# Optimization experiments

Measured on AMD Instinct MI355X. Metric: run time of the kernel, lower is better.

The kernel has to match this reference:

```python
import jax, jax.numpy as jnp
import numpy as np

B, T, D, E, H = 4, 2048, 1024, 4, 8
EPS = 1e-5


def _uniform(k, shape, bound):
    return jax.random.uniform(k, shape, jnp.float32, -bound, bound)


def setup_inputs() -> dict:
    key = jax.random.key(0)
    ks = jax.random.split(key, 12)
    wb = np.sqrt(6.0 / D) / np.sqrt(6.0)  # kaiming_uniform(a=sqrt5) bound ~ 1/sqrt(D)... keep simple
    wb = 1.0 / np.sqrt(D)
    return {
        "x": jax.random.normal(ks[0], (B, T, D), jnp.float32),
        "router_prob": jax.random.uniform(ks[1], (B, T, E), jnp.float32),
        "norm_w": jnp.ones((D,), jnp.float32),
        "norm_b": jnp.zeros((D,), jnp.float32),
        "q_w": _uniform(ks[2], (D, D), wb),
        "q_b": _uniform(ks[3], (D,), wb),
        "k_w": _uniform(ks[4], (D, D), wb),
        "k_b": _uniform(ks[5], (D,), wb),
        "v_w": _uniform(ks[6], (D, D), wb),
        "v_b": _uniform(ks[7], (D,), wb),
        "o_w": _uniform(ks[8], (D, D), wb),
        "o_b": _uniform(ks[9], (D,), wb),
    }


def _layernorm(x, w, b):
    mu = jnp.mean(x, axis=-1, keepdims=True)
    var = jnp.mean(jnp.square(x - mu), axis=-1, keepdims=True)
    return (x - mu) * jax.lax.rsqrt(var + EPS) * w + b


def reference(x, router_prob, norm_w, norm_b, q_w, q_b, k_w, k_b, v_w, v_b, o_w, o_b):
    e_cnt = router_prob.shape[2]
    b, t, d = x.shape
    n = t // e_cnt
    h = H
    scale = d ** (-0.5)  # note: original uses model_dim**-0.5, not head_dim

    qs, ks_, vs = [], [], []
    for e in range(e_cnt):
        xe = x[:, e * n:(e + 1) * n, :]
        xn = _layernorm(xe, norm_w, norm_b)
        m = d // (2 ** e)
        xm = xn[..., :m]  # [b, n, m] matryoshka slice
        # F.linear(xm, W[:, :m], bias): out = xm @ W[:, :m]^T + b -> [b, n, d]
        qs.append(jnp.einsum('bnm,dm->bnd', xm, q_w[:, :m]) + q_b)
        ks_.append(jnp.einsum('bnm,dm->bnd', xm, k_w[:, :m]) + k_b)
        vs.append(jnp.einsum('bnm,dm->bnd', xm, v_w[:, :m]) + v_b)
    q = jnp.concatenate(qs, axis=1)
    k = jnp.concatenate(ks_, axis=1)
    v = jnp.concatenate(vs, axis=1)

    dh = d // h
    q = q.reshape(b, t, h, dh).transpose(0, 2, 1, 3)  # b h t dh
    k = k.reshape(b, t, h, dh).transpose(0, 2, 1, 3)
    v = v.reshape(b, t, h, dh).transpose(0, 2, 1, 3)

    attn = jnp.einsum('bhqd,bhkd->bhqk', q, k) * scale
    attn = jax.nn.softmax(attn, axis=-1)  # dropout = identity in eval
    attn_out = jnp.einsum('bhqk,bhkd->bhqd', attn, v)
    attn_out = attn_out.transpose(0, 2, 1, 3).reshape(b, t, d)

    outs = []
    for e in range(e_cnt):
        sl = slice(e * n, (e + 1) * n)
        m = d // (2 ** e)
        xm = attn_out[:, sl, :m]
        out = jnp.einsum('bnm,om->bno', xm, o_w[:m, :m]) + o_b[:m]  # [b, n, m]
        pad = d - m
        if pad:
            out = jnp.pad(out, ((0, 0), (0, 0), (0, pad)))
        outs.append(out + x[:, sl, :])
    return jnp.concatenate(outs, axis=1)
```

## Files before the change

### kernel.cpp

```cpp
#include <hip/hip_runtime.h>
#include <hip/hip_bf16.h>

#define DEV static __device__ __forceinline__

typedef __attribute__((ext_vector_type(4))) float f32x4;
typedef __attribute__((ext_vector_type(8))) short s16x8;
typedef __attribute__((ext_vector_type(4))) unsigned int u32x4;

constexpr int Bn = 4, Tn = 2048, Dn = 1024, Hn = 8, DH = 128;
constexpr float EPSF = 1e-5f;
constexpr float QSCALE = 0.0450842200277801f;

DEV unsigned short f2bf(float f) {
    unsigned int u = __float_as_uint(f);
    u += 0x7FFF + ((u >> 16) & 1);
    return (unsigned short)(u >> 16);
}

DEV f32x4 mfma16(s16x8 a, s16x8 b, f32x4 c) {
    return __builtin_amdgcn_mfma_f32_16x16x32_bf16(a, b, c, 0, 0, 0);
}

DEV float ex2(float x) {
    float r;
    asm("v_exp_f32 %0, %1" : "=v"(r) : "v"(x));
    return r;
}

DEV unsigned int cvtpk(float lo, float hi) {
    unsigned int r;
    asm("v_cvt_pk_bf16_f32 %0, %1, %2" : "=v"(r) : "v"(lo), "v"(hi));
    return r;
}

typedef __attribute__((address_space(1))) const unsigned int GU32;
typedef __attribute__((address_space(3))) unsigned int LU32;
DEV void gload16(const void* g, void* l) {
    __builtin_amdgcn_global_load_lds((GU32*)g, (LU32*)l, 16, 0, 0);
}

__global__ void cvt_w_kernel(const float* __restrict__ qw, const float* __restrict__ kw,
                             const float* __restrict__ vw, const float* __restrict__ ow,
                             unsigned short* __restrict__ dst) {
    int idx = blockIdx.x * blockDim.x + threadIdx.x;
    const int total = 4 * Dn * Dn;
    for (; idx < total; idx += gridDim.x * blockDim.x) {
        int sel = idx >> 20;
        int off = idx & (Dn * Dn - 1);
        const float* src = sel == 0 ? qw : sel == 1 ? kw : sel == 2 ? vw : ow;
        dst[idx] = f2bf(src[off]);
    }
}

__global__ __launch_bounds__(256) void ln_kernel(const float* __restrict__ x,
                                                 const float* __restrict__ w,
                                                 const float* __restrict__ b,
                                                 unsigned short* __restrict__ xn) {
    int tok = blockIdx.x;
    int tid = threadIdx.x;
    const float* xp = x + (size_t)tok * Dn;
    float4 v = ((const float4*)xp)[tid];
    float s = v.x + v.y + v.z + v.w;
    float q = v.x * v.x + v.y * v.y + v.z * v.z + v.w * v.w;
    for (int off = 32; off; off >>= 1) {
        s += __shfl_xor(s, off);
        q += __shfl_xor(q, off);
    }
    __shared__ float red[8];
    __shared__ float stats[2];
    int wid = tid >> 6, lane = tid & 63;
    if (lane == 0) { red[wid] = s; red[4 + wid] = q; }
    __syncthreads();
    if (tid == 0) {
        float ts = red[0] + red[1] + red[2] + red[3];
        float tq = red[4] + red[5] + red[6] + red[7];
        float mu = ts / Dn;
        float var = tq / Dn - mu * mu;
        stats[0] = mu;
        stats[1] = rsqrtf(var + EPSF);
    }
    __syncthreads();
    float mu = stats[0], rs = stats[1];
    int c = tid * 4;
    ushort4 o;
    o.x = f2bf((v.x - mu) * rs * w[c + 0] + b[c + 0]);
    o.y = f2bf((v.y - mu) * rs * w[c + 1] + b[c + 1]);
    o.z = f2bf((v.z - mu) * rs * w[c + 2] + b[c + 2]);
    o.w = f2bf((v.w - mu) * rs * w[c + 3] + b[c + 3]);
    ((ushort4*)(xn + (size_t)tok * Dn))[tid] = o;
}

__global__ __launch_bounds__(256) void qkv_gemm(const unsigned short* __restrict__ xn,
                                                const unsigned short* __restrict__ wmat,
                                                const float* __restrict__ qb_,
                                                const float* __restrict__ kb_,
                                                const float* __restrict__ vb_,
                                                unsigned short* __restrict__ outq,
                                                unsigned short* __restrict__ outk,
                                                unsigned short* __restrict__ vt) {
    int rowbase = blockIdx.x * 128;
    int colbase = blockIdx.y * 128;
    int matid = blockIdx.z;
    const unsigned short* W = wmat + (size_t)matid * Dn * Dn;
    const float* bias = matid == 0 ? qb_ : matid == 1 ? kb_ : vb_;
    float oscale = matid == 0 ? QSCALE : 1.0f;
    int e = (rowbase & (Tn - 1)) >> 9;
    int m = Dn >> e;
    int nt = m >> 5;

    __shared__ alignas(16) unsigned short At[4][128 * 32];
    __shared__ alignas(16) unsigned short Bt[4][128 * 32];

    int tid = threadIdx.x;
    int lane = tid & 63, wv = tid >> 6;
    int wr = (wv >> 1) * 64, wc = (wv & 1) * 64;
    int fr = lane & 15, fg = lane >> 4;
    int srow = tid >> 2, scol = (tid & 3) * 8;
    const unsigned short* ga0 = xn + (size_t)(rowbase + srow) * Dn + scol;
    const unsigned short* ga1 = xn + (size_t)(rowbase + 64 + srow) * Dn + scol;
    const unsigned short* gb0 = W + (size_t)(colbase + srow) * Dn + scol;
    const unsigned short* gb1 = W + (size_t)(colbase + 64 + srow) * Dn + scol;

    f32x4 acc[4][4] = {};

    auto STAGE = [&](int tt) {
        int buf = tt & 3, kk = tt * 32;
        gload16(ga0 + kk, &At[buf][tid * 8]);
        gload16(ga1 + kk, &At[buf][2048 + tid * 8]);
        gload16(gb0 + kk, &Bt[buf][tid * 8]);
        gload16(gb1 + kk, &Bt[buf][2048 + tid * 8]);
    };

    STAGE(0);
    if (nt > 1) STAGE(1);

    for (int t = 0; t < nt; t++) {
        if (t + 1 < nt) { asm volatile("s_waitcnt vmcnt(4)" ::: "memory"); }
        else            { asm volatile("s_waitcnt vmcnt(0)" ::: "memory"); }
        __builtin_amdgcn_s_barrier();
        if (t + 2 < nt) STAGE(t + 2);
        int cur = t & 3;
        s16x8 a[4], b[4];
        #pragma unroll
        for (int i = 0; i < 4; i++) a[i] = *(const s16x8*)&At[cur][(wr + i * 16 + fr) * 32 + fg * 8];
        #pragma unroll
        for (int j = 0; j < 4; j++) b[j] = *(const s16x8*)&Bt[cur][(wc + j * 16 + fr) * 32 + fg * 8];
        #pragma unroll
        for (int i = 0; i < 4; i++)
            #pragma unroll
            for (int j = 0; j < 4; j++) acc[i][j] = mfma16(a[i], b[j], acc[i][j]);
    }

    if (matid == 2) {
        #pragma unroll
        for (int i = 0; i < 4; i++)
            #pragma unroll
            for (int j = 0; j < 4; j++) {
                int col = colbase + wc + j * 16 + fr;
                float bv = bias[col];
                int row0 = rowbase + wr + i * 16 + fg * 4;
                int bb = row0 >> 11, tl = row0 & (Tn - 1);
                int w32 = tl & 31;
                int tlp = (tl & ~31) | (((w32 >> 2) & 3) * 8 + ((w32 >> 4) & 1) * 4);
                size_t base = (((size_t)bb * Hn + (col >> 7)) * DH + (col & (DH - 1))) * Tn + tlp;
                ushort4 o;
                o.x = f2bf(acc[i][j][0] + bv);
                o.y = f2bf(acc[i][j][1] + bv);
                o.z = f2bf(acc[i][j][2] + bv);
                o.w = f2bf(acc[i][j][3] + bv);
                *(ushort4*)&vt[base] = o;
            }
    } else {
        unsigned short* out = matid == 0 ? outq : outk;
        #pragma unroll
        for (int i = 0; i < 4; i++)
            #pragma unroll
            for (int j = 0; j < 4; j++) {
                int col = colbase + wc + j * 16 + fr;
                float bv = bias[col];
                #pragma unroll
                for (int r = 0; r < 4; r++) {
                    int row = rowbase + wr + i * 16 + fg * 4 + r;
                    out[(size_t)row * Dn + col] = f2bf((acc[i][j][r] + bv) * oscale);
                }
            }
    }
}

__global__ __launch_bounds__(256, 2) void attn_kernel(const unsigned short* __restrict__ Q,
                                                      const unsigned short* __restrict__ K,
                                                      const unsigned short* __restrict__ VT,
                                                      unsigned short* __restrict__ AO) {
    int f = blockIdx.x;
    int qi = f >> 5;
    int bh = f & 31;
    int b = bh >> 3, h = bh & 7;
    int qbase = qi * 128;
    int tid = threadIdx.x;
    int wv = tid >> 6, lane = tid & 63;
    int fr = lane & 15, fg = lane >> 4;

    __shared__ alignas(16) unsigned short Kt[2][64 * 128];
    __shared__ alignas(16) unsigned short Vt[2][128 * 64];

    s16x8 bq[2][4];
    #pragma unroll
    for (int hh = 0; hh < 2; hh++) {
        const size_t qr = ((size_t)b * Tn + qbase + wv * 32 + hh * 16 + fr) * Dn + h * DH;
        #pragma unroll
        for (int c = 0; c < 4; c++) bq[hh][c] = *(const s16x8*)&Q[qr + c * 32 + fg * 8];
    }

    const s16x8 ones = {(short)0x3F80, (short)0x3F80, (short)0x3F80, (short)0x3F80,
                        (short)0x3F80, (short)0x3F80, (short)0x3F80, (short)0x3F80};

    f32x4 acc[2][9] = {};
    float m_run[2] = {-1e30f, -1e30f};

    const unsigned short* Kbase = K + (size_t)b * Tn * Dn + h * DH;
    const unsigned short* Vbase = VT + ((size_t)b * Hn + h) * DH * Tn;

    int k_row_lo = tid >> 4, k_chk = tid & 15;
    int v_row_lo = tid >> 3, v_chk = tid & 7;

    auto STAGE = [&](int t, int buf) {
        int kb = t * 64;
        #pragma unroll
        for (int p = 0; p < 4; p++) {
            int row = p * 16 + k_row_lo;
            int chunk = k_chk ^ (row & 7);
            gload16(Kbase + (size_t)(kb + row) * Dn + chunk * 8,
                    &Kt[buf][p * 2048 + tid * 8]);
        }
        #pragma unroll
        for (int p = 0; p < 4; p++) {
            int row = p * 32 + v_row_lo;
            int chunk = v_chk ^ (row & 7);
            gload16(Vbase + (size_t)row * Tn + kb + chunk * 8,
                    &Vt[buf][p * 2048 + tid * 8]);
        }
    };

    STAGE(0, 0);
    __syncthreads();

    for (int t = 0; t < Tn / 64; t++) {
        int cur = t & 1;
        if (t < Tn / 64 - 1) STAGE(t + 1, cur ^ 1);

        const unsigned short* KtC = &Kt[cur][0];
        const unsigned short* VtC = &Vt[cur][0];

        f32x4 s[2][4] = {};
        __builtin_amdgcn_s_setprio(1);
        #pragma unroll
        for (int c = 0; c < 4; c++) {
            #pragma unroll
            for (int kt = 0; kt < 4; kt++) {
                s16x8 ak = *(const s16x8*)&KtC[(kt * 16 + fr) * 128 +
                                               (((c * 4 + fg) ^ (fr & 7)) * 8)];
                s[0][kt] = mfma16(ak, bq[0][c], s[0][kt]);
                s[1][kt] = mfma16(ak, bq[1][c], s[1][kt]);
            }
        }
        __builtin_amdgcn_s_setprio(0);

        float mx[2];
        #pragma unroll
        for (int hh = 0; hh < 2; hh++) {
            float v = s[hh][0][0];
            #pragma unroll
            for (int kt = 0; kt < 4; kt++)
                #pragma unroll
                for (int r = 0; r < 4; r++) v = fmaxf(v, s[hh][kt][r]);
            v = fmaxf(v, __shfl_xor(v, 16));
            v = fmaxf(v, __shfl_xor(v, 32));
            mx[hh] = v;
        }

        if (!__all(mx[0] - m_run[0] <= 8.0f && mx[1] - m_run[1] <= 8.0f)) {
            #pragma unroll
            for (int hh = 0; hh < 2; hh++) {
                float mnew = fmaxf(m_run[hh], mx[hh]);
                float fsc = ex2(m_run[hh] - mnew);
                float fw[4];
                #pragma unroll
                for (int r = 0; r < 4; r++) fw[r] = __shfl(fsc, fg * 4 + r);
                #pragma unroll
                for (int n = 0; n < 9; n++)
                    #pragma unroll
                    for (int r = 0; r < 4; r++) acc[hh][n][r] *= fw[r];
                m_run[hh] = mnew;
            }
        }

        s16x8 pa[2][2];
        #pragma unroll
        for (int hh = 0; hh < 2; hh++) {
            float p[16];
            #pragma unroll
            for (int kt = 0; kt < 4; kt++)
                #pragma unroll
                for (int r = 0; r < 4; r++) p[kt * 4 + r] = ex2(s[hh][kt][r] - m_run[hh]);
            #pragma unroll
            for (int ks = 0; ks < 2; ks++) {
                u32x4 pw;
                pw.x = cvtpk(p[ks * 8 + 0], p[ks * 8 + 1]);
                pw.y = cvtpk(p[ks * 8 + 2], p[ks * 8 + 3]);
                pw.z = cvtpk(p[ks * 8 + 4], p[ks * 8 + 5]);
                pw.w = cvtpk(p[ks * 8 + 6], p[ks * 8 + 7]);
                pa[hh][ks] = __builtin_bit_cast(s16x8, pw);
            }
        }

        __builtin_amdgcn_s_setprio(1);
        #pragma unroll
        for (int ks = 0; ks < 2; ks++) {
            #pragma unroll
            for (int n = 0; n < 8; n++) {
                int row = n * 16 + fr;
                s16x8 bv = *(const s16x8*)&VtC[row * 64 +
                                               (((ks * 4 + fg) ^ (fr & 7)) * 8)];
                acc[0][n] = mfma16(pa[0][ks], bv, acc[0][n]);
                acc[1][n] = mfma16(pa[1][ks], bv, acc[1][n]);
            }
            acc[0][8] = mfma16(pa[0][ks], ones, acc[0][8]);
            acc[1][8] = mfma16(pa[1][ks], ones, acc[1][8]);
        }
        __builtin_amdgcn_s_setprio(0);
        __syncthreads();
    }

    #pragma unroll
    for (int hh = 0; hh < 2; hh++) {
        float rl[4];
        #pragma unroll
        for (int r = 0; r < 4; r++) rl[r] = 1.0f / acc[hh][8][r];
        size_t orow0 = ((size_t)b * Tn + qbase + wv * 32 + hh * 16) * Dn + h * DH;
        for (int n = 0; n < 8; n++)
            for (int r = 0; r < 4; r++) {
                float v = acc[hh][n][r] * rl[r];
                AO[orow0 + (size_t)(fg * 4 + r) * Dn + n * 16 + fr] = f2bf(v);
            }
    }
}

__global__ __launch_bounds__(256) void oproj_gemm(const unsigned short* __restrict__ A,
                                                  const unsigned short* __restrict__ W,
                                                  const float* __restrict__ bias,
                                                  const float* __restrict__ x,
                                                  float* __restrict__ out) {
    int rowbase = blockIdx.x * 128;
    int colbase = blockIdx.y * 128;
    int e = (rowbase & (Tn - 1)) >> 9;
    int m = Dn >> e;
    int tid = threadIdx.x;

    if (colbase >= m) {
        #pragma unroll
        for (int i = 0; i < 16; i++) {
            int idx = i * 256 + tid;
            int r = idx >> 5, c4 = (idx & 31) * 4;
            size_t g = (size_t)(rowbase + r) * Dn + colbase + c4;
            *(float4*)&out[g] = *(const float4*)&x[g];
        }
        return;
    }

    __shared__ alignas(16) unsigned short At[4][128 * 32];
    __shared__ alignas(16) unsigned short Bt[4][128 * 32];
    int lane = tid & 63, wv = tid >> 6;
    int wr = (wv >> 1) * 64, wc = (wv & 1) * 64;
    int fr = lane & 15, fg = lane >> 4;
    int srow = tid >> 2, scol = (tid & 3) * 8;
    const unsigned short* ga0 = A + (size_t)(rowbase + srow) * Dn + scol;
    const unsigned short* ga1 = A + (size_t)(rowbase + 64 + srow) * Dn + scol;
    const unsigned short* gb0 = W + (size_t)(colbase + srow) * Dn + scol;
    const unsigned short* gb1 = W + (size_t)(colbase + 64 + srow) * Dn + scol;
    int nt = m >> 5;

    f32x4 acc[4][4] = {};

    auto STAGE = [&](int tt) {
        int buf = tt & 3, kk = tt * 32;
        gload16(ga0 + kk, &At[buf][tid * 8]);
        gload16(ga1 + kk, &At[buf][2048 + tid * 8]);
        gload16(gb0 + kk, &Bt[buf][tid * 8]);
        gload16(gb1 + kk, &Bt[buf][2048 + tid * 8]);
    };

    STAGE(0);
    if (nt > 1) STAGE(1);

    for (int t = 0; t < nt; t++) {
        if (t + 1 < nt) { asm volatile("s_waitcnt vmcnt(4)" ::: "memory"); }
        else            { asm volatile("s_waitcnt vmcnt(0)" ::: "memory"); }
        __builtin_amdgcn_s_barrier();
        if (t + 2 < nt) STAGE(t + 2);
        int cur = t & 3;
        s16x8 a[4], b[4];
        #pragma unroll
        for (int i = 0; i < 4; i++) a[i] = *(const s16x8*)&At[cur][(wr + i * 16 + fr) * 32 + fg * 8];
        #pragma unroll
        for (int j = 0; j < 4; j++) b[j] = *(const s16x8*)&Bt[cur][(wc + j * 16 + fr) * 32 + fg * 8];
        #pragma unroll
        for (int i = 0; i < 4; i++)
            #pragma unroll
            for (int j = 0; j < 4; j++) acc[i][j] = mfma16(a[i], b[j], acc[i][j]);
    }

    #pragma unroll
    for (int i = 0; i < 4; i++)
        #pragma unroll
        for (int j = 0; j < 4; j++) {
            int col = colbase + wc + j * 16 + fr;
            float bv = bias[col];
            #pragma unroll
            for (int r = 0; r < 4; r++) {
                int row = rowbase + wr + i * 16 + fg * 4 + r;
                size_t g = (size_t)row * Dn + col;
                out[g] = acc[i][j][r] + bv + x[g];
            }
        }
}

extern "C" void kernel_launch(void* const* d_in, const int* in_sizes, int n_in,
                              void* d_out, int out_size, void* d_ws, size_t ws_size,
                              hipStream_t stream) {
    const float* x   = (const float*)d_in[0];
    const float* nw  = (const float*)d_in[2];
    const float* nb  = (const float*)d_in[3];
    const float* qw  = (const float*)d_in[4];
    const float* qb_ = (const float*)d_in[5];
    const float* kw  = (const float*)d_in[6];
    const float* kb_ = (const float*)d_in[7];
    const float* vw  = (const float*)d_in[8];
    const float* vb_ = (const float*)d_in[9];
    const float* ow  = (const float*)d_in[10];
    const float* ob_ = (const float*)d_in[11];
    float* out = (float*)d_out;

    unsigned short* ws = (unsigned short*)d_ws;
    const size_t NTOK = (size_t)Bn * Tn;
    unsigned short* xn = ws;
    unsigned short* qd = xn + NTOK * Dn;
    unsigned short* kd = qd + NTOK * Dn;
    unsigned short* vt = kd + NTOK * Dn;
    unsigned short* ao = vt + NTOK * Dn;
    unsigned short* wb = ao + NTOK * Dn;

    hipLaunchKernelGGL(cvt_w_kernel, dim3(4096), dim3(256), 0, stream, qw, kw, vw, ow, wb);
    hipLaunchKernelGGL(ln_kernel, dim3(NTOK), dim3(256), 0, stream, x, nw, nb, xn);
    hipLaunchKernelGGL(qkv_gemm, dim3(64, 8, 3), dim3(256), 0, stream,
                       xn, wb, qb_, kb_, vb_, qd, kd, vt);
    hipLaunchKernelGGL(attn_kernel, dim3(512), dim3(256), 0, stream, qd, kd, vt, ao);
    hipLaunchKernelGGL(oproj_gemm, dim3(64, 8), dim3(256), 0, stream,
                       ao, wb + (size_t)3 * Dn * Dn, ob_, x, out);
}
```

Before: 187.6 us.

## Shrink attention KV tile to 32 and GEMM ring buffers to three stages

```diff
diff --git a/kernel.cpp b/kernel.cpp
--- a/kernel.cpp
+++ b/kernel.cpp
@@ -108,8 +108,8 @@
     int m = Dn >> e;
     int nt = m >> 5;
 
-    __shared__ alignas(16) unsigned short At[4][128 * 32];
-    __shared__ alignas(16) unsigned short Bt[4][128 * 32];
+    __shared__ alignas(16) unsigned short At[3][128 * 32];
+    __shared__ alignas(16) unsigned short Bt[3][128 * 32];
 
     int tid = threadIdx.x;
     int lane = tid & 63, wv = tid >> 6;
@@ -123,23 +123,23 @@
 
     f32x4 acc[4][4] = {};
 
-    auto STAGE = [&](int tt) {
-        int buf = tt & 3, kk = tt * 32;
+    auto STAGE = [&](int tt, int buf) {
+        int kk = tt * 32;
         gload16(ga0 + kk, &At[buf][tid * 8]);
         gload16(ga1 + kk, &At[buf][2048 + tid * 8]);
         gload16(gb0 + kk, &Bt[buf][tid * 8]);
         gload16(gb1 + kk, &Bt[buf][2048 + tid * 8]);
     };
 
-    STAGE(0);
-    if (nt > 1) STAGE(1);
-
+    STAGE(0, 0);
+    if (nt > 1) STAGE(1, 1);
+
+    int cur = 0, nxt2 = 2;
     for (int t = 0; t < nt; t++) {
         if (t + 1 < nt) { asm volatile("s_waitcnt vmcnt(4)" ::: "memory"); }
         else            { asm volatile("s_waitcnt vmcnt(0)" ::: "memory"); }
         __builtin_amdgcn_s_barrier();
-        if (t + 2 < nt) STAGE(t + 2);
-        int cur = t & 3;
+        if (t + 2 < nt) STAGE(t + 2, nxt2);
         s16x8 a[4], b[4];
         #pragma unroll
         for (int i = 0; i < 4; i++) a[i] = *(const s16x8*)&At[cur][(wr + i * 16 + fr) * 32 + fg * 8];
@@ -149,6 +149,8 @@
         for (int i = 0; i < 4; i++)
             #pragma unroll
             for (int j = 0; j < 4; j++) acc[i][j] = mfma16(a[i], b[j], acc[i][j]);
+        cur = cur == 2 ? 0 : cur + 1;
+        nxt2 = nxt2 == 2 ? 0 : nxt2 + 1;
     }
 
     if (matid == 2) {
@@ -187,7 +189,7 @@
     }
 }
 
-__global__ __launch_bounds__(256, 2) void attn_kernel(const unsigned short* __restrict__ Q,
+__global__ __launch_bounds__(256, 4) void attn_kernel(const unsigned short* __restrict__ Q,
                                                       const unsigned short* __restrict__ K,
                                                       const unsigned short* __restrict__ VT,
                                                       unsigned short* __restrict__ AO) {
@@ -200,8 +202,8 @@
     int wv = tid >> 6, lane = tid & 63;
     int fr = lane & 15, fg = lane >> 4;
 
-    __shared__ alignas(16) unsigned short Kt[2][64 * 128];
-    __shared__ alignas(16) unsigned short Vt[2][128 * 64];
+    __shared__ alignas(16) unsigned short Kt[2][32 * 128];
+    __shared__ alignas(16) unsigned short Vt[2][64 * 64];
 
     s16x8 bq[2][4];
     #pragma unroll
@@ -221,22 +223,23 @@
     const unsigned short* Vbase = VT + ((size_t)b * Hn + h) * DH * Tn;
 
     int k_row_lo = tid >> 4, k_chk = tid & 15;
-    int v_row_lo = tid >> 3, v_chk = tid & 7;
+    int v_row_lo = tid >> 3, v_s = tid & 7;
 
     auto STAGE = [&](int t, int buf) {
-        int kb = t * 64;
-        #pragma unroll
-        for (int p = 0; p < 4; p++) {
+        int kb = t * 32;
+        #pragma unroll
+        for (int p = 0; p < 2; p++) {
             int row = p * 16 + k_row_lo;
             int chunk = k_chk ^ (row & 7);
             gload16(Kbase + (size_t)(kb + row) * Dn + chunk * 8,
                     &Kt[buf][p * 2048 + tid * 8]);
         }
         #pragma unroll
-        for (int p = 0; p < 4; p++) {
+        for (int p = 0; p < 2; p++) {
             int row = p * 32 + v_row_lo;
-            int chunk = v_chk ^ (row & 7);
-            gload16(Vbase + (size_t)row * Tn + kb + chunk * 8,
+            int c = v_s ^ (row & 7);
+            int hi = c >> 2, fgc = c & 3;
+            gload16(Vbase + (size_t)(hi * 64 + row) * Tn + kb + fgc * 8,
                     &Vt[buf][p * 2048 + tid * 8]);
         }
     };
@@ -244,19 +247,19 @@
     STAGE(0, 0);
     __syncthreads();
 
-    for (int t = 0; t < Tn / 64; t++) {
+    for (int t = 0; t < Tn / 32; t++) {
         int cur = t & 1;
-        if (t < Tn / 64 - 1) STAGE(t + 1, cur ^ 1);
+        if (t < Tn / 32 - 1) STAGE(t + 1, cur ^ 1);
 
         const unsigned short* KtC = &Kt[cur][0];
         const unsigned short* VtC = &Vt[cur][0];
 
-        f32x4 s[2][4] = {};
+        f32x4 s[2][2] = {};
         __builtin_amdgcn_s_setprio(1);
         #pragma unroll
         for (int c = 0; c < 4; c++) {
             #pragma unroll
-            for (int kt = 0; kt < 4; kt++) {
+            for (int kt = 0; kt < 2; kt++) {
                 s16x8 ak = *(const s16x8*)&KtC[(kt * 16 + fr) * 128 +
                                                (((c * 4 + fg) ^ (fr & 7)) * 8)];
                 s[0][kt] = mfma16(ak, bq[0][c], s[0][kt]);
@@ -270,7 +273,7 @@
         for (int hh = 0; hh < 2; hh++) {
             float v = s[hh][0][0];
             #pragma unroll
-            for (int kt = 0; kt < 4; kt++)
+            for (int kt = 0; kt < 2; kt++)
                 #pragma unroll
                 for (int r = 0; r < 4; r++) v = fmaxf(v, s[hh][kt][r]);
             v = fmaxf(v, __shfl_xor(v, 16));
@@ -294,39 +297,34 @@
             }
         }
 
-        s16x8 pa[2][2];
+        s16x8 pa[2];
         #pragma unroll
         for (int hh = 0; hh < 2; hh++) {
-            float p[16];
-            #pragma unroll
-            for (int kt = 0; kt < 4; kt++)
+            float p[8];
+            #pragma unroll
+            for (int kt = 0; kt < 2; kt++)
                 #pragma unroll
                 for (int r = 0; r < 4; r++) p[kt * 4 + r] = ex2(s[hh][kt][r] - m_run[hh]);
-            #pragma unroll
-            for (int ks = 0; ks < 2; ks++) {
-                u32x4 pw;
-                pw.x = cvtpk(p[ks * 8 + 0], p[ks * 8 + 1]);
-                pw.y = cvtpk(p[ks * 8 + 2], p[ks * 8 + 3]);
-                pw.z = cvtpk(p[ks * 8 + 4], p[ks * 8 + 5]);
-                pw.w = cvtpk(p[ks * 8 + 6], p[ks * 8 + 7]);
-                pa[hh][ks] = __builtin_bit_cast(s16x8, pw);
-            }
+            u32x4 pw;
+            pw.x = cvtpk(p[0], p[1]);
+            pw.y = cvtpk(p[2], p[3]);
+            pw.z = cvtpk(p[4], p[5]);
+            pw.w = cvtpk(p[6], p[7]);
+            pa[hh] = __builtin_bit_cast(s16x8, pw);
         }
 
         __builtin_amdgcn_s_setprio(1);
         #pragma unroll
-        for (int ks = 0; ks < 2; ks++) {
-            #pragma unroll
-            for (int n = 0; n < 8; n++) {
-                int row = n * 16 + fr;
-                s16x8 bv = *(const s16x8*)&VtC[row * 64 +
-                                               (((ks * 4 + fg) ^ (fr & 7)) * 8)];
-                acc[0][n] = mfma16(pa[0][ks], bv, acc[0][n]);
-                acc[1][n] = mfma16(pa[1][ks], bv, acc[1][n]);
-            }
-            acc[0][8] = mfma16(pa[0][ks], ones, acc[0][8]);
-            acc[1][8] = mfma16(pa[1][ks], ones, acc[1][8]);
-        }
+        for (int n = 0; n < 8; n++) {
+            int row = (n & 3) * 16 + fr;
+            int hi = n >> 2;
+            s16x8 bv = *(const s16x8*)&VtC[row * 64 +
+                                           (((hi * 4 + fg) ^ (row & 7)) * 8)];
+            acc[0][n] = mfma16(pa[0], bv, acc[0][n]);
+            acc[1][n] = mfma16(pa[1], bv, acc[1][n]);
+        }
+        acc[0][8] = mfma16(pa[0], ones, acc[0][8]);
+        acc[1][8] = mfma16(pa[1], ones, acc[1][8]);
         __builtin_amdgcn_s_setprio(0);
         __syncthreads();
     }
@@ -367,8 +365,8 @@
         return;
     }
 
-    __shared__ alignas(16) unsigned short At[4][128 * 32];
-    __shared__ alignas(16) unsigned short Bt[4][128 * 32];
+    __shared__ alignas(16) unsigned short At[3][128 * 32];
+    __shared__ alignas(16) unsigned short Bt[3][128 * 32];
     int lane = tid & 63, wv = tid >> 6;
     int wr = (wv >> 1) * 64, wc = (wv & 1) * 64;
     int fr = lane & 15, fg = lane >> 4;
@@ -381,23 +379,23 @@
 
     f32x4 acc[4][4] = {};
 
-    auto STAGE = [&](int tt) {
-        int buf = tt & 3, kk = tt * 32;
+    auto STAGE = [&](int tt, int buf) {
+        int kk = tt * 32;
         gload16(ga0 + kk, &At[buf][tid * 8]);
         gload16(ga1 + kk, &At[buf][2048 + tid * 8]);
         gload16(gb0 + kk, &Bt[buf][tid * 8]);
         gload16(gb1 + kk, &Bt[buf][2048 + tid * 8]);
     };
 
-    STAGE(0);
-    if (nt > 1) STAGE(1);
-
+    STAGE(0, 0);
+    if (nt > 1) STAGE(1, 1);
+
+    int cur = 0, nxt2 = 2;
     for (int t = 0; t < nt; t++) {
         if (t + 1 < nt) { asm volatile("s_waitcnt vmcnt(4)" ::: "memory"); }
         else            { asm volatile("s_waitcnt vmcnt(0)" ::: "memory"); }
         __builtin_amdgcn_s_barrier();
-        if (t + 2 < nt) STAGE(t + 2);
-        int cur = t & 3;
+        if (t + 2 < nt) STAGE(t + 2, nxt2);
         s16x8 a[4], b[4];
         #pragma unroll
         for (int i = 0; i < 4; i++) a[i] = *(const s16x8*)&At[cur][(wr + i * 16 + fr) * 32 + fg * 8];
@@ -407,6 +405,8 @@
         for (int i = 0; i < 4; i++)
             #pragma unroll
             for (int j = 0; j < 4; j++) acc[i][j] = mfma16(a[i], b[j], acc[i][j]);
+        cur = cur == 2 ? 0 : cur + 1;
+        nxt2 = nxt2 == 2 ? 0 : nxt2 + 1;
     }
 
     #pragma unroll
```

New measurement: 288.1 us. 53.6% more time.

## Software-pipeline attention: overlap next tile QK^T with current softmax/PV

Applied to the files above, without the earlier changes.

```diff
diff --git a/kernel.cpp b/kernel.cpp
--- a/kernel.cpp
+++ b/kernel.cpp
@@ -201,7 +201,7 @@
     int fr = lane & 15, fg = lane >> 4;
 
     __shared__ alignas(16) unsigned short Kt[2][64 * 128];
-    __shared__ alignas(16) unsigned short Vt[2][128 * 64];
+    __shared__ alignas(16) unsigned short Vt[3][128 * 64];
 
     s16x8 bq[2][4];
     #pragma unroll
@@ -223,61 +223,61 @@
     int k_row_lo = tid >> 4, k_chk = tid & 15;
     int v_row_lo = tid >> 3, v_chk = tid & 7;
 
-    auto STAGE = [&](int t, int buf) {
+    auto STAGE = [&](int t) {
         int kb = t * 64;
+        int kbuf = t & 1, vbuf = t % 3;
         #pragma unroll
         for (int p = 0; p < 4; p++) {
             int row = p * 16 + k_row_lo;
             int chunk = k_chk ^ (row & 7);
             gload16(Kbase + (size_t)(kb + row) * Dn + chunk * 8,
-                    &Kt[buf][p * 2048 + tid * 8]);
+                    &Kt[kbuf][p * 2048 + tid * 8]);
         }
         #pragma unroll
         for (int p = 0; p < 4; p++) {
             int row = p * 32 + v_row_lo;
             int chunk = v_chk ^ (row & 7);
             gload16(Vbase + (size_t)row * Tn + kb + chunk * 8,
-                    &Vt[buf][p * 2048 + tid * 8]);
-        }
-    };
-
-    STAGE(0, 0);
-    __syncthreads();
-
-    for (int t = 0; t < Tn / 64; t++) {
-        int cur = t & 1;
-        if (t < Tn / 64 - 1) STAGE(t + 1, cur ^ 1);
-
-        const unsigned short* KtC = &Kt[cur][0];
-        const unsigned short* VtC = &Vt[cur][0];
-
-        f32x4 s[2][4] = {};
-        __builtin_amdgcn_s_setprio(1);
+                    &Vt[vbuf][p * 2048 + tid * 8]);
+        }
+    };
+
+    auto SYNC = [&]() {
+        asm volatile("s_waitcnt vmcnt(0)" ::: "memory");
+        __builtin_amdgcn_s_barrier();
+    };
+
+    auto QKT = [&](int t, f32x4 (&sN)[2][4]) {
+        const unsigned short* KtC = &Kt[t & 1][0];
+        #pragma unroll
+        for (int hh = 0; hh < 2; hh++)
+            #pragma unroll
+            for (int kt = 0; kt < 4; kt++) sN[hh][kt] = f32x4{0.f, 0.f, 0.f, 0.f};
         #pragma unroll
         for (int c = 0; c < 4; c++) {
             #pragma unroll
             for (int kt = 0; kt < 4; kt++) {
                 s16x8 ak = *(const s16x8*)&KtC[(kt * 16 + fr) * 128 +
                                                (((c * 4 + fg) ^ (fr & 7)) * 8)];
-                s[0][kt] = mfma16(ak, bq[0][c], s[0][kt]);
-                s[1][kt] = mfma16(ak, bq[1][c], s[1][kt]);
-            }
-        }
-        __builtin_amdgcn_s_setprio(0);
-
+                sN[0][kt] = mfma16(ak, bq[0][c], sN[0][kt]);
+                sN[1][kt] = mfma16(ak, bq[1][c], sN[1][kt]);
+            }
+        }
+    };
+
+    auto SMPV = [&](int tp, f32x4 (&sO)[2][4]) {
         float mx[2];
         #pragma unroll
         for (int hh = 0; hh < 2; hh++) {
-            float v = s[hh][0][0];
+            float v = sO[hh][0][0];
             #pragma unroll
             for (int kt = 0; kt < 4; kt++)
                 #pragma unroll
-                for (int r = 0; r < 4; r++) v = fmaxf(v, s[hh][kt][r]);
+                for (int r = 0; r < 4; r++) v = fmaxf(v, sO[hh][kt][r]);
             v = fmaxf(v, __shfl_xor(v, 16));
             v = fmaxf(v, __shfl_xor(v, 32));
             mx[hh] = v;
         }
-
         if (!__all(mx[0] - m_run[0] <= 8.0f && mx[1] - m_run[1] <= 8.0f)) {
             #pragma unroll
             for (int hh = 0; hh < 2; hh++) {
@@ -293,7 +293,6 @@
                 m_run[hh] = mnew;
             }
         }
-
         s16x8 pa[2][2];
         #pragma unroll
         for (int hh = 0; hh < 2; hh++) {
@@ -301,7 +300,7 @@
             #pragma unroll
             for (int kt = 0; kt < 4; kt++)
                 #pragma unroll
-                for (int r = 0; r < 4; r++) p[kt * 4 + r] = ex2(s[hh][kt][r] - m_run[hh]);
+                for (int r = 0; r < 4; r++) p[kt * 4 + r] = ex2(sO[hh][kt][r] - m_run[hh]);
             #pragma unroll
             for (int ks = 0; ks < 2; ks++) {
                 u32x4 pw;
@@ -312,7 +311,7 @@
                 pa[hh][ks] = __builtin_bit_cast(s16x8, pw);
             }
         }
-
+        const unsigned short* VtC = &Vt[tp % 3][0];
         __builtin_amdgcn_s_setprio(1);
         #pragma unroll
         for (int ks = 0; ks < 2; ks++) {
@@ -328,8 +327,30 @@
             acc[1][8] = mfma16(pa[1][ks], ones, acc[1][8]);
         }
         __builtin_amdgcn_s_setprio(0);
-        __syncthreads();
-    }
+    };
+
+    f32x4 sA[2][4], sB[2][4];
+
+    STAGE(0);
+    SYNC();
+    STAGE(1);
+    QKT(0, sA);
+    SYNC();
+    STAGE(2);
+
+    for (int t = 1; t < 31; t += 2) {
+        QKT(t, sB);
+        SMPV(t - 1, sA);
+        SYNC();
+        if (t + 2 < 32) STAGE(t + 2);
+        QKT(t + 1, sA);
+        SMPV(t, sB);
+        SYNC();
+        if (t + 3 < 32) STAGE(t + 3);
+    }
+    QKT(31, sB);
+    SMPV(30, sA);
+    SMPV(31, sB);
 
     #pragma unroll
     for (int hh = 0; hh < 2; hh++) {
```

Result: no change. 188.1 us (+0.2%).

## Give each attention wave 64 query rows and shrink GEMM LDS ring to three

Applied to the files above, without the earlier changes.

```diff
diff --git a/kernel.cpp b/kernel.cpp
--- a/kernel.cpp
+++ b/kernel.cpp
@@ -108,8 +108,8 @@
     int m = Dn >> e;
     int nt = m >> 5;
 
-    __shared__ alignas(16) unsigned short At[4][128 * 32];
-    __shared__ alignas(16) unsigned short Bt[4][128 * 32];
+    __shared__ alignas(16) unsigned short At[3][128 * 32];
+    __shared__ alignas(16) unsigned short Bt[3][128 * 32];
 
     int tid = threadIdx.x;
     int lane = tid & 63, wv = tid >> 6;
@@ -123,23 +123,23 @@
 
     f32x4 acc[4][4] = {};
 
-    auto STAGE = [&](int tt) {
-        int buf = tt & 3, kk = tt * 32;
+    auto STAGE = [&](int tt, int buf) {
+        int kk = tt * 32;
         gload16(ga0 + kk, &At[buf][tid * 8]);
         gload16(ga1 + kk, &At[buf][2048 + tid * 8]);
         gload16(gb0 + kk, &Bt[buf][tid * 8]);
         gload16(gb1 + kk, &Bt[buf][2048 + tid * 8]);
     };
 
-    STAGE(0);
-    if (nt > 1) STAGE(1);
-
+    STAGE(0, 0);
+    if (nt > 1) STAGE(1, 1);
+
+    int cur = 0, nxt2 = 2;
     for (int t = 0; t < nt; t++) {
         if (t + 1 < nt) { asm volatile("s_waitcnt vmcnt(4)" ::: "memory"); }
         else            { asm volatile("s_waitcnt vmcnt(0)" ::: "memory"); }
         __builtin_amdgcn_s_barrier();
-        if (t + 2 < nt) STAGE(t + 2);
-        int cur = t & 3;
+        if (t + 2 < nt) STAGE(t + 2, nxt2);
         s16x8 a[4], b[4];
         #pragma unroll
         for (int i = 0; i < 4; i++) a[i] = *(const s16x8*)&At[cur][(wr + i * 16 + fr) * 32 + fg * 8];
@@ -149,6 +149,8 @@
         for (int i = 0; i < 4; i++)
             #pragma unroll
             for (int j = 0; j < 4; j++) acc[i][j] = mfma16(a[i], b[j], acc[i][j]);
+        cur = cur == 2 ? 0 : cur + 1;
+        nxt2 = nxt2 == 2 ? 0 : nxt2 + 1;
     }
 
     if (matid == 2) {
@@ -187,7 +189,7 @@
     }
 }
 
-__global__ __launch_bounds__(256, 2) void attn_kernel(const unsigned short* __restrict__ Q,
+__global__ __launch_bounds__(128, 1) void attn_kernel(const unsigned short* __restrict__ Q,
                                                       const unsigned short* __restrict__ K,
                                                       const unsigned short* __restrict__ VT,
                                                       unsigned short* __restrict__ AO) {
@@ -203,10 +205,10 @@
     __shared__ alignas(16) unsigned short Kt[2][64 * 128];
     __shared__ alignas(16) unsigned short Vt[2][128 * 64];
 
-    s16x8 bq[2][4];
+    s16x8 bq[4][4];
     #pragma unroll
-    for (int hh = 0; hh < 2; hh++) {
-        const size_t qr = ((size_t)b * Tn + qbase + wv * 32 + hh * 16 + fr) * Dn + h * DH;
+    for (int hh = 0; hh < 4; hh++) {
+        const size_t qr = ((size_t)b * Tn + qbase + wv * 64 + hh * 16 + fr) * Dn + h * DH;
         #pragma unroll
         for (int c = 0; c < 4; c++) bq[hh][c] = *(const s16x8*)&Q[qr + c * 32 + fg * 8];
     }
@@ -214,8 +216,8 @@
     const s16x8 ones = {(short)0x3F80, (short)0x3F80, (short)0x3F80, (short)0x3F80,
                         (short)0x3F80, (short)0x3F80, (short)0x3F80, (short)0x3F80};
 
-    f32x4 acc[2][9] = {};
-    float m_run[2] = {-1e30f, -1e30f};
+    f32x4 acc[4][9] = {};
+    float m_run[4] = {-1e30f, -1e30f, -1e30f, -1e30f};
 
     const unsigned short* Kbase = K + (size_t)b * Tn * Dn + h * DH;
     const unsigned short* Vbase = VT + ((size_t)b * Hn + h) * DH * Tn;
@@ -226,18 +228,18 @@
     auto STAGE = [&](int t, int buf) {
         int kb = t * 64;
         #pragma unroll
-        for (int p = 0; p < 4; p++) {
-            int row = p * 16 + k_row_lo;
+        for (int p = 0; p < 8; p++) {
+            int row = p * 8 + k_row_lo;
             int chunk = k_chk ^ (row & 7);
             gload16(Kbase + (size_t)(kb + row) * Dn + chunk * 8,
-                    &Kt[buf][p * 2048 + tid * 8]);
-        }
-        #pragma unroll
-        for (int p = 0; p < 4; p++) {
-            int row = p * 32 + v_row_lo;
+                    &Kt[buf][p * 1024 + tid * 8]);
+        }
+        #pragma unroll
+        for (int p = 0; p < 8; p++) {
+            int row = p * 16 + v_row_lo;
             int chunk = v_chk ^ (row & 7);
             gload16(Vbase + (size_t)row * Tn + kb + chunk * 8,
-                    &Vt[buf][p * 2048 + tid * 8]);
+                    &Vt[buf][p * 1024 + tid * 8]);
         }
     };
 
@@ -251,7 +253,7 @@
         const unsigned short* KtC = &Kt[cur][0];
         const unsigned short* VtC = &Vt[cur][0];
 
-        f32x4 s[2][4] = {};
+        f32x4 s[4][4] = {};
         __builtin_amdgcn_s_setprio(1);
         #pragma unroll
         for (int c = 0; c < 4; c++) {
@@ -259,15 +261,16 @@
             for (int kt = 0; kt < 4; kt++) {
                 s16x8 ak = *(const s16x8*)&KtC[(kt * 16 + fr) * 128 +
                                                (((c * 4 + fg) ^ (fr & 7)) * 8)];
-                s[0][kt] = mfma16(ak, bq[0][c], s[0][kt]);
-                s[1][kt] = mfma16(ak, bq[1][c], s[1][kt]);
+                #pragma unroll
+                for (int hh = 0; hh < 4; hh++)
+                    s[hh][kt] = mfma16(ak, bq[hh][c], s[hh][kt]);
             }
         }
         __builtin_amdgcn_s_setprio(0);
 
-        float mx[2];
-        #pragma unroll
-        for (int hh = 0; hh < 2; hh++) {
+        float mx[4];
+        #pragma unroll
+        for (int hh = 0; hh < 4; hh++) {
             float v = s[hh][0][0];
             #pragma unroll
             for (int kt = 0; kt < 4; kt++)
@@ -278,9 +281,11 @@
             mx[hh] = v;
         }
 
-        if (!__all(mx[0] - m_run[0] <= 8.0f && mx[1] - m_run[1] <= 8.0f)) {
-            #pragma unroll
-            for (int hh = 0; hh < 2; hh++) {
+        bool ok = (mx[0] - m_run[0] <= 8.0f) && (mx[1] - m_run[1] <= 8.0f) &&
+                  (mx[2] - m_run[2] <= 8.0f) && (mx[3] - m_run[3] <= 8.0f);
+        if (!__all(ok)) {
+            #pragma unroll
+            for (int hh = 0; hh < 4; hh++) {
                 float mnew = fmaxf(m_run[hh], mx[hh]);
                 float fsc = ex2(m_run[hh] - mnew);
                 float fw[4];
@@ -294,9 +299,9 @@
             }
         }
 
-        s16x8 pa[2][2];
-        #pragma unroll
-        for (int hh = 0; hh < 2; hh++) {
+        s16x8 pa[4][2];
+        #pragma unroll
+        for (int hh = 0; hh < 4; hh++) {
             float p[16];
             #pragma unroll
             for (int kt = 0; kt < 4; kt++)
@@ -321,22 +326,24 @@
                 int row = n * 16 + fr;
                 s16x8 bv = *(const s16x8*)&VtC[row * 64 +
                                                (((ks * 4 + fg) ^ (fr & 7)) * 8)];
-                acc[0][n] = mfma16(pa[0][ks], bv, acc[0][n]);
-                acc[1][n] = mfma16(pa[1][ks], bv, acc[1][n]);
-            }
-            acc[0][8] = mfma16(pa[0][ks], ones, acc[0][8]);
-            acc[1][8] = mfma16(pa[1][ks], ones, acc[1][8]);
+                #pragma unroll
+                for (int hh = 0; hh < 4; hh++)
+                    acc[hh][n] = mfma16(pa[hh][ks], bv, acc[hh][n]);
+            }
+            #pragma unroll
+            for (int hh = 0; hh < 4; hh++)
+                acc[hh][8] = mfma16(pa[hh][ks], ones, acc[hh][8]);
         }
         __builtin_amdgcn_s_setprio(0);
         __syncthreads();
     }
 
     #pragma unroll
-    for (int hh = 0; hh < 2; hh++) {
+    for (int hh = 0; hh < 4; hh++) {
         float rl[4];
         #pragma unroll
         for (int r = 0; r < 4; r++) rl[r] = 1.0f / acc[hh][8][r];
-        size_t orow0 = ((size_t)b * Tn + qbase + wv * 32 + hh * 16) * Dn + h * DH;
+        size_t orow0 = ((size_t)b * Tn + qbase + wv * 64 + hh * 16) * Dn + h * DH;
         for (int n = 0; n < 8; n++)
             for (int r = 0; r < 4; r++) {
                 float v = acc[hh][n][r] * rl[r];
@@ -367,8 +374,8 @@
         return;
     }
 
-    __shared__ alignas(16) unsigned short At[4][128 * 32];
-    __shared__ alignas(16) unsigned short Bt[4][128 * 32];
+    __shared__ alignas(16) unsigned short At[3][128 * 32];
+    __shared__ alignas(16) unsigned short Bt[3][128 * 32];
     int lane = tid & 63, wv = tid >> 6;
     int wr = (wv >> 1) * 64, wc = (wv & 1) * 64;
     int fr = lane & 15, fg = lane >> 4;
@@ -381,23 +388,23 @@
 
     f32x4 acc[4][4] = {};
 
-    auto STAGE = [&](int tt) {
-        int buf = tt & 3, kk = tt * 32;
+    auto STAGE = [&](int tt, int buf) {
+        int kk = tt * 32;
         gload16(ga0 + kk, &At[buf][tid * 8]);
         gload16(ga1 + kk, &At[buf][2048 + tid * 8]);
         gload16(gb0 + kk, &Bt[buf][tid * 8]);
         gload16(gb1 + kk, &Bt[buf][2048 + tid * 8]);
     };
 
-    STAGE(0);
-    if (nt > 1) STAGE(1);
-
+    STAGE(0, 0);
+    if (nt > 1) STAGE(1, 1);
+
+    int cur = 0, nxt2 = 2;
     for (int t = 0; t < nt; t++) {
         if (t + 1 < nt) { asm volatile("s_waitcnt vmcnt(4)" ::: "memory"); }
         else            { asm volatile("s_waitcnt vmcnt(0)" ::: "memory"); }
         __builtin_amdgcn_s_barrier();
-        if (t + 2 < nt) STAGE(t + 2);
-        int cur = t & 3;
+        if (t + 2 < nt) STAGE(t + 2, nxt2);
         s16x8 a[4], b[4];
         #pragma unroll
         for (int i = 0; i < 4; i++) a[i] = *(const s16x8*)&At[cur][(wr + i * 16 + fr) * 32 + fg * 8];
@@ -407,6 +414,8 @@
         for (int i = 0; i < 4; i++)
             #pragma unroll
             for (int j = 0; j < 4; j++) acc[i][j] = mfma16(a[i], b[j], acc[i][j]);
+        cur = cur == 2 ? 0 : cur + 1;
+        nxt2 = nxt2 == 2 ? 0 : nxt2 + 1;
     }
 
     #pragma unroll
@@ -453,7 +462,7 @@
     hipLaunchKernelGGL(ln_kernel, dim3(NTOK), dim3(256), 0, stream, x, nw, nb, xn);
     hipLaunchKernelGGL(qkv_gemm, dim3(64, 8, 3), dim3(256), 0, stream,
                        xn, wb, qb_, kb_, vb_, qd, kd, vt);
-    hipLaunchKernelGGL(attn_kernel, dim3(512), dim3(256), 0, stream, qd, kd, vt, ao);
+    hipLaunchKernelGGL(attn_kernel, dim3(512), dim3(128), 0, stream, qd, kd, vt, ao);
     hipLaunchKernelGGL(oproj_gemm, dim3(64, 8), dim3(256), 0, stream,
                        ao, wb + (size_t)3 * Dn * Dn, ob_, x, out);
 }
```

Measured after the change: 225.5 us. 1.2x slower.
